# Performance work log

Measured on AMD Instinct MI355X. Metric: run time of the kernel, lower is better.

## Reference

```python
import jax, jax.numpy as jnp
import numpy as np

N_SYS, N_ANC = 2, 2
NQ = N_SYS + N_ANC          # 4 qubits total
DIM = 2 ** NQ               # 16-dim statevector
NUM_LAYERS = 2

# --- constant gate structure (PennyLane convention: wire 0 is the MSB) ---

def _cnot_full(control, target):
    U = np.zeros((DIM, DIM), dtype=np.float32)
    for i in range(DIM):
        cbit = (i >> (NQ - 1 - control)) & 1
        j = i ^ ((1 << (NQ - 1 - target)) * cbit)
        U[j, i] = 1.0
    return U

# BasicEntanglerLayers ring: CNOT(0,1), CNOT(1,2), CNOT(2,3), CNOT(3,0) in sequence
_ring = np.eye(DIM, dtype=np.float32)
for _c in range(NQ):
    _ring = _cnot_full(_c, (_c + 1) % NQ) @ _ring
CNOT_RING = jnp.asarray(_ring)

# PauliZ eigenvalues on measurement_qubit = 1 (second-most-significant wire)
_Z1 = jnp.asarray(np.array([(-1.0) ** ((i >> (NQ - 2)) & 1) for i in range(DIM)],
                            dtype=np.float32))

# --- parameterized part ---

def _ry(theta):
    # RY is real: [[cos t/2, -sin t/2], [sin t/2, cos t/2]]
    c, s = jnp.cos(theta * 0.5), jnp.sin(theta * 0.5)
    return jnp.stack([jnp.stack([c, -s]), jnp.stack([s, c])])

def _layer_unitary(w):
    # one BasicEntangler layer: RY(w[q]) on each wire, then the CNOT ring
    U = _ry(w[0])
    for q in range(1, NQ):
        U = jnp.kron(U, _ry(w[q]))
    return CNOT_RING @ U

def _circuit_unitary(U_params, Udagger_params):
    # entangling layers (0,1) then 'disentangling' with layer order flipped (1,0)
    weights = jnp.concatenate([U_params, Udagger_params[::-1]], axis=0)  # (4, NQ)
    C = jnp.eye(DIM, dtype=U_params.dtype)
    for l in range(2 * NUM_LAYERS):
        C = _layer_unitary(weights[l]) @ C
    return C


def setup_inputs() -> dict:
    key = jax.random.key(0)
    k1, k2, k3, k4, k5, k6 = jax.random.split(key, 6)
    B = 1048576
    return {
        "x": jax.random.normal(k1, (B, 1), dtype=jnp.float32),
        "h_prev": jax.random.uniform(k2, (B, 4), dtype=jnp.float32),
        "W_in": jax.random.normal(k3, (4, 1), dtype=jnp.float32),
        "b_in": jax.random.normal(k4, (4,), dtype=jnp.float32),
        "U_params": jax.random.uniform(k5, (2, 4), dtype=jnp.float32),
        "Udagger_params": jax.random.uniform(k6, (2, 4), dtype=jnp.float32),
    }


def reference(x, h_prev, W_in, b_in, U_params, Udagger_params):
    B = x.shape[0]
    # input projection + normalization (replicates proj / ||proj + 1e-12||)
    proj = x @ W_in.T + b_in                                   # (B, 4)
    inp = proj / jnp.linalg.norm(proj + 1e-12, axis=-1, keepdims=True)
    # AmplitudeEmbedding(kron(input_state, h_prev), normalize=True)
    joint = (inp[:, :, None] * h_prev[:, None, :]).reshape(B, DIM)   # (B, 16)
    joint = joint / jnp.linalg.norm(joint, axis=-1, keepdims=True)
    # all gates (RY, CNOT) are real -> state stays real; fuse circuit into one 16x16
    C = _circuit_unitary(U_params, Udagger_params)
    psi = joint @ C.T                                          # (B, 16)
    p = psi * psi                                              # |amplitude|^2
    # diag of reduced density matrix on ancilla wires [2,3]: trace out system wires
    h_next = p.reshape(B, 2 ** N_SYS, 2 ** N_ANC).sum(axis=1)  # (B, 4)
    # expval PauliZ(wire 1)
    output = p @ _Z1                                           # (B,)
    return h_next, output
```

## Files before the change

### kernel.cpp

```cpp
#include <hip/hip_runtime.h>


__device__ __forceinline__ int ring_perm(int k) {
  int b0 = (k >> 3) & 1, b1 = (k >> 2) & 1, b2 = (k >> 1) & 1, b3 = k & 1;
  b1 ^= b0; b2 ^= b1; b3 ^= b2; b0 ^= b3;
  return (b0 << 3) | (b1 << 2) | (b2 << 1) | b3;
}

__global__ __launch_bounds__(256) void build_consts_kernel(
    const float* __restrict__ W_in, const float* __restrict__ b_in,
    const float* __restrict__ U, const float* __restrict__ Ud,
    float* __restrict__ ws) {
  __shared__ float M[16][16];
  __shared__ float Lm[16][16];
  const int t = threadIdx.x;
  const int i = t >> 4, j = t & 15;
  const int pi = ring_perm(i);

  float ang[4][4];
#pragma unroll
  for (int q = 0; q < 4; ++q) {
    ang[0][q] = U[q];
    ang[1][q] = U[4 + q];
    ang[2][q] = Ud[4 + q];
    ang[3][q] = Ud[q];
  }

  {
    float kel = 1.f;
#pragma unroll
    for (int q = 0; q < 4; ++q) {
      float c = cosf(0.5f * ang[0][q]);
      float s = sinf(0.5f * ang[0][q]);
      int iq = (i >> (3 - q)) & 1, jq = (j >> (3 - q)) & 1;
      kel *= (iq == jq) ? c : (iq ? s : -s);
    }
    M[pi][j] = kel;
  }
  __syncthreads();

  for (int l = 1; l < 4; ++l) {
    float kel = 1.f;
#pragma unroll
    for (int q = 0; q < 4; ++q) {
      float c = cosf(0.5f * ang[l][q]);
      float s = sinf(0.5f * ang[l][q]);
      int iq = (i >> (3 - q)) & 1, jq = (j >> (3 - q)) & 1;
      kel *= (iq == jq) ? c : (iq ? s : -s);
    }
    Lm[pi][j] = kel;
    __syncthreads();
    float acc = 0.f;
#pragma unroll
    for (int k = 0; k < 16; ++k) acc += Lm[i][k] * M[k][j];
    __syncthreads();
    M[i][j] = acc;
    __syncthreads();
  }

  if (t < 64) {
    const int r = t >> 2, k = t & 3;
    float a = 0.f, bb = 0.f;
#pragma unroll
    for (int q = 0; q < 4; ++q) {
      float c = M[r][4 * q + k];
      a = fmaf(W_in[q], c, a);
      bb = fmaf(b_in[q], c, bb);
    }
    ws[r * 4 + k] = a;
    ws[64 + r * 4 + k] = bb;
  }
  if (t == 0) {
    float qa = 0.f, qb = 0.f, qc = 0.f;
#pragma unroll
    for (int q = 0; q < 4; ++q) {
      qa = fmaf(W_in[q], W_in[q], qa);
      qb = fmaf(2.f * W_in[q], b_in[q], qb);
      qc = fmaf(b_in[q], b_in[q], qc);
    }
    ws[128] = qa; ws[129] = qb; ws[130] = qc;
  }
}

__global__ __launch_bounds__(256) void qlstm_kernel(
    const float* __restrict__ x, const float4* __restrict__ h_prev,
    const float* __restrict__ AB, float4* __restrict__ h_next,
    float* __restrict__ outp, int B) {
  int gid = blockIdx.x * 256 + threadIdx.x;
  if (gid >= B) return;
  float xv = x[gid];
  float4 h = h_prev[gid];
  float nh2 = fmaf(h.x, h.x, fmaf(h.y, h.y, fmaf(h.z, h.z, h.w * h.w)));
  float qa = AB[128], qb = AB[129], qc = AB[130];
  float nu2 = fmaf(fmaf(qa, xv, qb), xv, qc);
  float inv2 = __builtin_amdgcn_rcpf(nu2 * nh2);

  float hn[4] = {0.f, 0.f, 0.f, 0.f};
  float po = 0.f;
#pragma unroll
  for (int r = 0; r < 16; ++r) {
    float ar = fmaf(AB[r * 4 + 0], h.x,
               fmaf(AB[r * 4 + 1], h.y,
               fmaf(AB[r * 4 + 2], h.z, AB[r * 4 + 3] * h.w)));
    float br = fmaf(AB[64 + r * 4 + 0], h.x,
               fmaf(AB[64 + r * 4 + 1], h.y,
               fmaf(AB[64 + r * 4 + 2], h.z, AB[64 + r * 4 + 3] * h.w)));
    float tr = fmaf(xv, ar, br);
    float s = tr * tr;
    hn[r & 3] += s;
    po += ((r >> 2) & 1) ? -s : s;
  }
  float4 o;
  o.x = hn[0] * inv2;
  o.y = hn[1] * inv2;
  o.z = hn[2] * inv2;
  o.w = hn[3] * inv2;
  h_next[gid] = o;
  outp[gid] = po * inv2;
}

extern "C" void kernel_launch(void* const* d_in, const int* in_sizes, int n_in,
                              void* d_out, int out_size, void* d_ws, size_t ws_size,
                              hipStream_t stream) {
  const float* x  = (const float*)d_in[0];
  const float* h  = (const float*)d_in[1];
  const float* W  = (const float*)d_in[2];
  const float* bi = (const float*)d_in[3];
  const float* U  = (const float*)d_in[4];
  const float* Ud = (const float*)d_in[5];
  float* ws = (float*)d_ws;
  const int B = in_sizes[0];
  float* h_next = (float*)d_out;
  float* out1   = (float*)d_out + 4 * (size_t)B;

  build_consts_kernel<<<1, 256, 0, stream>>>(W, bi, U, Ud, ws);
  qlstm_kernel<<<(B + 255) / 256, 256, 0, stream>>>(
      x, (const float4*)h, ws, (float4*)h_next, out1, B);
}
```

Baseline: 87.23 us.

## Fuse constant build into main kernel and process four rows per thread

Drops the separate single-block setup kernel. Every block now builds the 16x16 circuit unitary and the projection coefficients itself in shared memory, then processes four batch rows per thread with float4 loads of x and a float4 store of the output. This removes one kernel launch and its serialization and cuts the grid by four. In exchange every block redundantly recomputes the trig and the three matrix products behind several barriers, which adds a fixed prologue to each of roughly 1024 blocks.

```diff
diff --git a/kernel.cpp b/kernel.cpp
--- a/kernel.cpp
+++ b/kernel.cpp
@@ -7,116 +7,171 @@
   return (b0 << 3) | (b1 << 2) | (b2 << 1) | b3;
 }
 
-__global__ __launch_bounds__(256) void build_consts_kernel(
+__global__ __launch_bounds__(256) void qlstm_fused_kernel(
+    const float* __restrict__ x, const float4* __restrict__ h_prev,
     const float* __restrict__ W_in, const float* __restrict__ b_in,
     const float* __restrict__ U, const float* __restrict__ Ud,
-    float* __restrict__ ws) {
+    float4* __restrict__ h_next, float* __restrict__ outp, int B) {
   __shared__ float M[16][16];
   __shared__ float Lm[16][16];
+  __shared__ float AB[132];
+
   const int t = threadIdx.x;
-  const int i = t >> 4, j = t & 15;
-  const int pi = ring_perm(i);
+  {
+    const int i = t >> 4, j = t & 15;
+    const int pi = ring_perm(i);
 
-  float ang[4][4];
-#pragma unroll
-  for (int q = 0; q < 4; ++q) {
-    ang[0][q] = U[q];
-    ang[1][q] = U[4 + q];
-    ang[2][q] = Ud[4 + q];
-    ang[3][q] = Ud[q];
-  }
-
-  {
-    float kel = 1.f;
+    float ang[4][4];
 #pragma unroll
     for (int q = 0; q < 4; ++q) {
-      float c = cosf(0.5f * ang[0][q]);
-      float s = sinf(0.5f * ang[0][q]);
-      int iq = (i >> (3 - q)) & 1, jq = (j >> (3 - q)) & 1;
-      kel *= (iq == jq) ? c : (iq ? s : -s);
+      ang[0][q] = U[q];
+      ang[1][q] = U[4 + q];
+      ang[2][q] = Ud[4 + q];
+      ang[3][q] = Ud[q];
     }
-    M[pi][j] = kel;
-  }
-  __syncthreads();
 
-  for (int l = 1; l < 4; ++l) {
-    float kel = 1.f;
+    {
+      float kel = 1.f;
 #pragma unroll
-    for (int q = 0; q < 4; ++q) {
-      float c = cosf(0.5f * ang[l][q]);
-      float s = sinf(0.5f * ang[l][q]);
-      int iq = (i >> (3 - q)) & 1, jq = (j >> (3 - q)) & 1;
-      kel *= (iq == jq) ? c : (iq ? s : -s);
+      for (int q = 0; q < 4; ++q) {
+        float c = cosf(0.5f * ang[0][q]);
+        float s = sinf(0.5f * ang[0][q]);
+        int iq = (i >> (3 - q)) & 1, jq = (j >> (3 - q)) & 1;
+        kel *= (iq == jq) ? c : (iq ? s : -s);
+      }
+      M[pi][j] = kel;
     }
-    Lm[pi][j] = kel;
     __syncthreads();
-    float acc = 0.f;
+
+    for (int l = 1; l < 4; ++l) {
+      float kel = 1.f;
 #pragma unroll
-    for (int k = 0; k < 16; ++k) acc += Lm[i][k] * M[k][j];
-    __syncthreads();
-    M[i][j] = acc;
+      for (int q = 0; q < 4; ++q) {
+        float c = cosf(0.5f * ang[l][q]);
+        float s = sinf(0.5f * ang[l][q]);
+        int iq = (i >> (3 - q)) & 1, jq = (j >> (3 - q)) & 1;
+        kel *= (iq == jq) ? c : (iq ? s : -s);
+      }
+      Lm[pi][j] = kel;
+      __syncthreads();
+      float acc = 0.f;
+#pragma unroll
+      for (int k = 0; k < 16; ++k) acc += Lm[i][k] * M[k][j];
+      __syncthreads();
+      M[i][j] = acc;
+      __syncthreads();
+    }
+
+    if (t < 64) {
+      const int r = t >> 2, k = t & 3;
+      float a = 0.f, bb = 0.f;
+#pragma unroll
+      for (int q = 0; q < 4; ++q) {
+        float c = M[r][4 * q + k];
+        a = fmaf(W_in[q], c, a);
+        bb = fmaf(b_in[q], c, bb);
+      }
+      AB[r * 4 + k] = a;
+      AB[64 + r * 4 + k] = bb;
+    }
+    if (t == 0) {
+      float qa = 0.f, qb = 0.f, qc = 0.f;
+#pragma unroll
+      for (int q = 0; q < 4; ++q) {
+        qa = fmaf(W_in[q], W_in[q], qa);
+        qb = fmaf(2.f * W_in[q], b_in[q], qb);
+        qc = fmaf(b_in[q], b_in[q], qc);
+      }
+      AB[128] = qa; AB[129] = qb; AB[130] = qc;
+    }
     __syncthreads();
   }
 
-  if (t < 64) {
-    const int r = t >> 2, k = t & 3;
-    float a = 0.f, bb = 0.f;
+  const int gid = blockIdx.x * 256 + t;
+  const int row0 = gid * 4;
+  if (row0 >= B) return;
+
+  const float qa = AB[128], qb = AB[129], qc = AB[130];
+
+  if (row0 + 3 < B) {
+    float4 xv4 = ((const float4*)x)[gid];
+    float xv[4] = {xv4.x, xv4.y, xv4.z, xv4.w};
+    float4 h[4];
 #pragma unroll
-    for (int q = 0; q < 4; ++q) {
-      float c = M[r][4 * q + k];
-      a = fmaf(W_in[q], c, a);
-      bb = fmaf(b_in[q], c, bb);
+    for (int m = 0; m < 4; ++m) h[m] = h_prev[row0 + m];
+
+    float inv2[4];
+#pragma unroll
+    for (int m = 0; m < 4; ++m) {
+      float nh2 = fmaf(h[m].x, h[m].x,
+                  fmaf(h[m].y, h[m].y,
+                  fmaf(h[m].z, h[m].z, h[m].w * h[m].w)));
+      float nu2 = fmaf(fmaf(qa, xv[m], qb), xv[m], qc);
+      inv2[m] = __builtin_amdgcn_rcpf(nu2 * nh2);
     }
-    ws[r * 4 + k] = a;
-    ws[64 + r * 4 + k] = bb;
+
+    float hn[4][4] = {};
+    float po[4] = {0.f, 0.f, 0.f, 0.f};
+#pragma unroll
+    for (int r = 0; r < 16; ++r) {
+      const float a0 = AB[r * 4 + 0], a1 = AB[r * 4 + 1];
+      const float a2 = AB[r * 4 + 2], a3 = AB[r * 4 + 3];
+      const float b0 = AB[64 + r * 4 + 0], b1 = AB[64 + r * 4 + 1];
+      const float b2 = AB[64 + r * 4 + 2], b3 = AB[64 + r * 4 + 3];
+#pragma unroll
+      for (int m = 0; m < 4; ++m) {
+        float ar = fmaf(a0, h[m].x, fmaf(a1, h[m].y, fmaf(a2, h[m].z, a3 * h[m].w)));
+        float br = fmaf(b0, h[m].x, fmaf(b1, h[m].y, fmaf(b2, h[m].z, b3 * h[m].w)));
+        float tr = fmaf(xv[m], ar, br);
+        float s = tr * tr;
+        hn[m][r & 3] += s;
+        po[m] += ((r >> 2) & 1) ? -s : s;
+      }
+    }
+
+#pragma unroll
+    for (int m = 0; m < 4; ++m) {
+      float4 o;
+      o.x = hn[m][0] * inv2[m];
+      o.y = hn[m][1] * inv2[m];
+      o.z = hn[m][2] * inv2[m];
+      o.w = hn[m][3] * inv2[m];
+      h_next[row0 + m] = o;
+    }
+    float4 po4;
+    po4.x = po[0] * inv2[0]; po4.y = po[1] * inv2[1];
+    po4.z = po[2] * inv2[2]; po4.w = po[3] * inv2[3];
+    ((float4*)outp)[gid] = po4;
+  } else {
+    for (int m = 0; m < 4 && row0 + m < B; ++m) {
+      const int row = row0 + m;
+      float xv = x[row];
+      float4 h = h_prev[row];
+      float nh2 = fmaf(h.x, h.x, fmaf(h.y, h.y, fmaf(h.z, h.z, h.w * h.w)));
+      float nu2 = fmaf(fmaf(qa, xv, qb), xv, qc);
+      float inv2 = __builtin_amdgcn_rcpf(nu2 * nh2);
+      float hn[4] = {0.f, 0.f, 0.f, 0.f};
+      float po = 0.f;
+#pragma unroll
+      for (int r = 0; r < 16; ++r) {
+        float ar = fmaf(AB[r * 4 + 0], h.x,
+                   fmaf(AB[r * 4 + 1], h.y,
+                   fmaf(AB[r * 4 + 2], h.z, AB[r * 4 + 3] * h.w)));
+        float br = fmaf(AB[64 + r * 4 + 0], h.x,
+                   fmaf(AB[64 + r * 4 + 1], h.y,
+                   fmaf(AB[64 + r * 4 + 2], h.z, AB[64 + r * 4 + 3] * h.w)));
+        float tr = fmaf(xv, ar, br);
+        float s = tr * tr;
+        hn[r & 3] += s;
+        po += ((r >> 2) & 1) ? -s : s;
+      }
+      float4 o;
+      o.x = hn[0] * inv2; o.y = hn[1] * inv2;
+      o.z = hn[2] * inv2; o.w = hn[3] * inv2;
+      h_next[row] = o;
+      outp[row] = po * inv2;
+    }
   }
-  if (t == 0) {
-    float qa = 0.f, qb = 0.f, qc = 0.f;
-#pragma unroll
-    for (int q = 0; q < 4; ++q) {
-      qa = fmaf(W_in[q], W_in[q], qa);
-      qb = fmaf(2.f * W_in[q], b_in[q], qb);
-      qc = fmaf(b_in[q], b_in[q], qc);
-    }
-    ws[128] = qa; ws[129] = qb; ws[130] = qc;
-  }
-}
-
-__global__ __launch_bounds__(256) void qlstm_kernel(
-    const float* __restrict__ x, const float4* __restrict__ h_prev,
-    const float* __restrict__ AB, float4* __restrict__ h_next,
-    float* __restrict__ outp, int B) {
-  int gid = blockIdx.x * 256 + threadIdx.x;
-  if (gid >= B) return;
-  float xv = x[gid];
-  float4 h = h_prev[gid];
-  float nh2 = fmaf(h.x, h.x, fmaf(h.y, h.y, fmaf(h.z, h.z, h.w * h.w)));
-  float qa = AB[128], qb = AB[129], qc = AB[130];
-  float nu2 = fmaf(fmaf(qa, xv, qb), xv, qc);
-  float inv2 = __builtin_amdgcn_rcpf(nu2 * nh2);
-
-  float hn[4] = {0.f, 0.f, 0.f, 0.f};
-  float po = 0.f;
-#pragma unroll
-  for (int r = 0; r < 16; ++r) {
-    float ar = fmaf(AB[r * 4 + 0], h.x,
-               fmaf(AB[r * 4 + 1], h.y,
-               fmaf(AB[r * 4 + 2], h.z, AB[r * 4 + 3] * h.w)));
-    float br = fmaf(AB[64 + r * 4 + 0], h.x,
-               fmaf(AB[64 + r * 4 + 1], h.y,
-               fmaf(AB[64 + r * 4 + 2], h.z, AB[64 + r * 4 + 3] * h.w)));
-    float tr = fmaf(xv, ar, br);
-    float s = tr * tr;
-    hn[r & 3] += s;
-    po += ((r >> 2) & 1) ? -s : s;
-  }
-  float4 o;
-  o.x = hn[0] * inv2;
-  o.y = hn[1] * inv2;
-  o.z = hn[2] * inv2;
-  o.w = hn[3] * inv2;
-  h_next[gid] = o;
-  outp[gid] = po * inv2;
 }
 
 extern "C" void kernel_launch(void* const* d_in, const int* in_sizes, int n_in,
@@ -128,12 +183,12 @@
   const float* bi = (const float*)d_in[3];
   const float* U  = (const float*)d_in[4];
   const float* Ud = (const float*)d_in[5];
-  float* ws = (float*)d_ws;
   const int B = in_sizes[0];
   float* h_next = (float*)d_out;
   float* out1   = (float*)d_out + 4 * (size_t)B;
 
-  build_consts_kernel<<<1, 256, 0, stream>>>(W, bi, U, Ud, ws);
-  qlstm_kernel<<<(B + 255) / 256, 256, 0, stream>>>(
-      x, (const float4*)h, ws, (float4*)h_next, out1, B);
+  const int nthreads = (B + 3) / 4;
+  const int grid = (nthreads + 255) / 256;
+  qlstm_fused_kernel<<<grid, 256, 0, stream>>>(
+      x, (const float4*)h, W, bi, U, Ud, (float4*)h_next, out1, B);
 }
```

After: 91.85 us. 1.05x slower.
